# Kernel optimization log

Measured on AMD Instinct MI355X. Metric: run time of the kernel, lower is better.

Reference implementation:

```python
import jax, jax.numpy as jnp
import numpy as np

NH = 12  # attention heads (bert-base)


def _ln(x, s, b, eps=1e-12):
    mu = x.mean(-1, keepdims=True)
    var = ((x - mu) ** 2).mean(-1, keepdims=True)
    return (x - mu) / jnp.sqrt(var + eps) * s + b


def _forward(input_ids, token_type_ids, attention_mask, word_emb, pos_emb, type_emb,
             emb_ln_s, emb_ln_b, memory, q_w, q_b, k_w, k_b, v_w, v_b, o_w, o_b,
             ln1_s, ln1_b, f_w1, f_b1, f_w2, f_b2, ln2_s, ln2_b,
             key_w1, key_b1, key_w2, key_b2, val_w1, val_b1, val_w2, val_b2):
    B, S = input_ids.shape
    M, H = memory.shape
    T = S + M
    m = attention_mask.astype(jnp.int32)          # [B,S] 0/1
    L = m.sum(-1)                                 # [B] number of real tokens
    tok_emb = word_emb[input_ids]                 # [B,S,H]
    # stable argsort puts mask==1 positions first (in original order), then mask==0
    order = jnp.argsort(1 - m, axis=-1)           # [B,S]
    p = jnp.arange(T)[None, :]                    # [1,T]
    Lb = L[:, None]
    # output layout per sample: [real tokens (L), memory (M), pad tokens (S-L)]
    src_p = jnp.clip(jnp.where(p < Lb, p, p - M), 0, S - 1)
    src_idx = jnp.take_along_axis(order, src_p, axis=1)                  # [B,T]
    gathered = jnp.take_along_axis(tok_emb, src_idx[..., None], axis=1)  # [B,T,H]
    is_mem = (p >= Lb) & (p < Lb + M)
    mem_idx = jnp.clip(p - Lb, 0, M - 1)
    emb = jnp.where(is_mem[..., None], memory[mem_idx], gathered)        # spliced embeds
    att = (p < Lb + M).astype(emb.dtype)                                 # [B,T]
    tt = jnp.where(p < Lb, jnp.take_along_axis(token_type_ids.astype(jnp.int32), src_idx, axis=1), 1)
    # --- BERT encoder on inputs_embeds ---
    x = _ln(emb + pos_emb[None, :T] + type_emb[tt], emb_ln_s, emb_ln_b)
    bias = ((1.0 - att) * -10000.0)[:, None, None, :]                    # [B,1,1,T]
    dh = H // NH
    for l in range(q_w.shape[0]):
        q = (x @ q_w[l] + q_b[l]).reshape(B, T, NH, dh)
        k = (x @ k_w[l] + k_b[l]).reshape(B, T, NH, dh)
        v = (x @ v_w[l] + v_b[l]).reshape(B, T, NH, dh)
        s = jnp.einsum('bqhd,bkhd->bhqk', q, k) / jnp.sqrt(jnp.asarray(dh, x.dtype)) + bias
        a = jax.nn.softmax(s, axis=-1)
        ctx = jnp.einsum('bhqk,bkhd->bqhd', a, v).reshape(B, T, H)
        x = _ln(x + ctx @ o_w[l] + o_b[l], ln1_s[l], ln1_b[l])
        h = jax.nn.gelu(x @ f_w1[l] + f_b1[l], approximate=False)
        x = _ln(x + h @ f_w2[l] + f_b2[l], ln2_s[l], ln2_b[l])
    # --- gated key/value softmax pooling (get_rep_no_vae) ---
    value = jnp.tanh(jax.nn.relu(x @ val_w1 + val_b1) @ val_w2 + val_b2)       # [B,T,E]
    weight = jax.nn.sigmoid(jax.nn.relu(x @ key_w1 + key_b1) @ key_w2 + key_b2)  # [B,T,E]
    pool_mask = jnp.where(tt == 1, -jnp.inf, 0.0).astype(x.dtype)[..., None]   # [B,T,1]
    fw = jax.nn.softmax(weight + pool_mask, axis=-2)  # softmax over token dim
    return jax.nn.relu((fw * value).sum(-2))          # [B,E]


def setup_inputs() -> dict:
    key = jax.random.key(0)
    ks = jax.random.split(key, 20)
    B, S, M, H, E, V, NL, FF = 8, 512, 64, 768, 512, 30522, 2, 3072
    def rn(k, shape, s=0.02):
        return jax.random.normal(k, shape, jnp.float32) * s
    return {
        'input_ids': jax.random.randint(ks[0], (B, S), 0, V),
        'token_type_ids': jnp.zeros((B, S), jnp.int32),
        'attention_mask': jax.random.randint(ks[1], (B, S), 0, 2),
        'word_emb': rn(ks[2], (V, H)),
        'pos_emb': rn(ks[3], (S + M, H)),
        'type_emb': rn(ks[4], (2, H)),
        'emb_ln_s': jnp.ones((H,), jnp.float32), 'emb_ln_b': jnp.zeros((H,), jnp.float32),
        'memory': rn(ks[5], (M, H), 1.0),
        'q_w': rn(ks[6], (NL, H, H)), 'q_b': jnp.zeros((NL, H), jnp.float32),
        'k_w': rn(ks[7], (NL, H, H)), 'k_b': jnp.zeros((NL, H), jnp.float32),
        'v_w': rn(ks[8], (NL, H, H)), 'v_b': jnp.zeros((NL, H), jnp.float32),
        'o_w': rn(ks[9], (NL, H, H)), 'o_b': jnp.zeros((NL, H), jnp.float32),
        'ln1_s': jnp.ones((NL, H), jnp.float32), 'ln1_b': jnp.zeros((NL, H), jnp.float32),
        'f_w1': rn(ks[10], (NL, H, FF)), 'f_b1': jnp.zeros((NL, FF), jnp.float32),
        'f_w2': rn(ks[11], (NL, FF, H)), 'f_b2': jnp.zeros((NL, H), jnp.float32),
        'ln2_s': jnp.ones((NL, H), jnp.float32), 'ln2_b': jnp.zeros((NL, H), jnp.float32),
        'key_w1': rn(ks[12], (H, 2 * H)), 'key_b1': jnp.zeros((2 * H,), jnp.float32),
        'key_w2': rn(ks[13], (2 * H, E)), 'key_b2': jnp.zeros((E,), jnp.float32),
        'val_w1': rn(ks[14], (H, 2 * E)), 'val_b1': jnp.zeros((2 * E,), jnp.float32),
        'val_w2': rn(ks[15], (2 * E, E)), 'val_b2': jnp.zeros((E,), jnp.float32),
    }


def reference(input_ids, token_type_ids, attention_mask, word_emb, pos_emb, type_emb,
              emb_ln_s, emb_ln_b, memory, q_w, q_b, k_w, k_b, v_w, v_b, o_w, o_b,
              ln1_s, ln1_b, f_w1, f_b1, f_w2, f_b2, ln2_s, ln2_b,
              key_w1, key_b1, key_w2, key_b2, val_w1, val_b1, val_w2, val_b2):
    return _forward(input_ids, token_type_ids, attention_mask, word_emb, pos_emb, type_emb,
                    emb_ln_s, emb_ln_b, memory, q_w, q_b, k_w, k_b, v_w, v_b, o_w, o_b,
                    ln1_s, ln1_b, f_w1, f_b1, f_w2, f_b2, ln2_s, ln2_b,
                    key_w1, key_b1, key_w2, key_b2, val_w1, val_b1, val_w2, val_b2)
```

## Files before the change

kernel.cpp:

```cpp
#include <hip/hip_runtime.h>
#include <hip/hip_bf16.h>

#define B 8
#define S 512
#define MM 64
#define T 576
#define H 768
#define NH 12
#define DH 64
#define FF 3072
#define E 512
#define NL 2

typedef __attribute__((ext_vector_type(8))) short bf16x8;
typedef __attribute__((ext_vector_type(4))) float f32x4;

__device__ inline unsigned short bf16_rne(float f) {
    unsigned u = __builtin_bit_cast(unsigned, f);
    unsigned r = u + 0x7FFFu + ((u >> 16) & 1u);
    return (unsigned short)(r >> 16);
}

__device__ inline f32x4 mfma16(bf16x8 a, bf16x8 b, f32x4 c) {
    return __builtin_amdgcn_mfma_f32_16x16x32_bf16(a, b, c, 0, 0, 0);
}

__device__ inline void load_lds16(const void* g, void* l) {
    __builtin_amdgcn_global_load_lds((const __attribute__((address_space(1))) void*)g,
                                     (__attribute__((address_space(3))) void*)l, 16, 0, 0);
}

__global__ void order_kernel(const int* __restrict__ mask, int* __restrict__ ord,
                             int* __restrict__ Larr) {
    __shared__ int ps[S];
    int b = blockIdx.x;
    int t = threadIdx.x;
    int mv = (mask[b * S + t] != 0) ? 1 : 0;
    ps[t] = mv;
    __syncthreads();
    for (int off = 1; off < S; off <<= 1) {
        int v = ps[t];
        int add = (t >= off) ? ps[t - off] : 0;
        __syncthreads();
        ps[t] = v + add;
        __syncthreads();
    }
    int L = ps[S - 1];
    int rank = mv ? (ps[t] - 1) : (L + (t - ps[t]));
    ord[b * S + rank] = t;
    if (t == 0) Larr[b] = L;
}

__global__ void scan_kernel(const int* __restrict__ Larr, int* __restrict__ boff,
                            int* __restrict__ rowb) {
    __shared__ int sb[B + 1];
    if (threadIdx.x == 0) {
        int acc = 0;
        for (int b = 0; b < B; ++b) { sb[b] = acc; boff[b] = acc; acc += Larr[b] + MM; }
        sb[B] = acc; boff[B] = acc;
    }
    __syncthreads();
    for (int r = threadIdx.x; r < B * T; r += blockDim.x) {
        int bb = 0;
        #pragma unroll
        for (int b2 = 1; b2 < B; ++b2) bb += (r >= sb[b2]) ? 1 : 0;
        rowb[r] = bb;
    }
}

__global__ void embed_kernel(const int* __restrict__ ids, const int* __restrict__ toktype,
                             const int* __restrict__ ord, const int* __restrict__ Larr,
                             const int* __restrict__ boff,
                             const float* __restrict__ word_emb, const float* __restrict__ pos_emb,
                             const float* __restrict__ type_emb, const float* __restrict__ memory,
                             const float* __restrict__ lns, const float* __restrict__ lnb,
                             float* __restrict__ x, unsigned short* __restrict__ xb,
                             int* __restrict__ ttarr) {
    int t = blockIdx.x;
    int b = blockIdx.y;
    int Lb = Larr[b];
    if (t >= Lb + MM) return;
    int row = boff[b] + t;
    int tid = threadIdx.x;
    int tt;
    const float* src;
    if (t < Lb) {
        int sp = ord[b * S + t];
        tt = toktype[b * S + sp];
        src = &word_emb[(size_t)ids[b * S + sp] * H];
    } else {
        tt = 1;
        src = &memory[(size_t)(t - Lb) * H];
    }
    __shared__ float rowv[H];
    __shared__ float r1[256], r2[256];
    float lsum = 0.f, lsq = 0.f;
    for (int hh = tid; hh < H; hh += 256) {
        float v = src[hh] + pos_emb[(size_t)t * H + hh] + type_emb[(size_t)tt * H + hh];
        rowv[hh] = v;
        lsum += v;
        lsq += v * v;
    }
    r1[tid] = lsum; r2[tid] = lsq;
    __syncthreads();
    for (int s = 128; s > 0; s >>= 1) {
        if (tid < s) { r1[tid] += r1[tid + s]; r2[tid] += r2[tid + s]; }
        __syncthreads();
    }
    float mu = r1[0] / H;
    float var = r2[0] / H - mu * mu;
    float inv = rsqrtf(var + 1e-12f);
    for (int hh = tid; hh < H; hh += 256) {
        float v = (rowv[hh] - mu) * inv * lns[hh] + lnb[hh];
        x[(size_t)row * H + hh] = v;
        xb[(size_t)row * H + hh] = bf16_rne(v);
    }
    if (tid == 0) ttarr[row] = tt;
}

#define ACT_NONE 0
#define ACT_RELU 1
#define ACT_GELU 2
#define ACT_SIGMOID 3
#define ACT_TANH 4

template <int ACT>
__device__ inline float apply_act(float v) {
    if constexpr (ACT == ACT_RELU) return fmaxf(v, 0.f);
    else if constexpr (ACT == ACT_GELU) {
        float y = v * 0.70710678118654752f;
        float a = fabsf(y);
        float t = 1.f / (1.f + 0.3275911f * a);
        float poly = t * (0.254829592f + t * (-0.284496736f + t * (1.421413741f +
                     t * (-1.453152027f + t * 1.061405429f))));
        float e = poly * exp2f(-a * a * 1.4426950408889634f);
        float erfv = 1.f - e;
        erfv = (y < 0.f) ? -erfv : erfv;
        return 0.5f * v * (1.f + erfv);
    }
    else if constexpr (ACT == ACT_SIGMOID) return 1.f / (1.f + expf(-v));
    else if constexpr (ACT == ACT_TANH) return tanhf(v);
    else return v;
}

struct TDesc { const float* src; unsigned dstoff; int Kd; int Nd; int tile0; };
struct TTab { TDesc d[10]; int n; };

__global__ __launch_bounds__(256) void transpose_all(TTab tab, unsigned short* __restrict__ dstbase) {
    int tile = blockIdx.x;
    int mi = 0;
    #pragma unroll
    for (int i = 1; i < 10; ++i)
        if (i < tab.n && tab.d[i].tile0 <= tile) mi = i;
    TDesc d = tab.d[mi];
    int rel = tile - d.tile0;
    int tilesK = d.Kd >> 5;
    int kt = rel % tilesK, nt = rel / tilesK;
    __shared__ float ts[32][33];
    int k0 = kt * 32, n0 = nt * 32;
    int tx = threadIdx.x & 31, ty = threadIdx.x >> 5;
    #pragma unroll
    for (int r = 0; r < 4; ++r) {
        int kk = ty + r * 8;
        ts[kk][tx] = d.src[(size_t)(k0 + kk) * d.Nd + n0 + tx];
    }
    __syncthreads();
    unsigned short* Wt = dstbase + d.dstoff;
    #pragma unroll
    for (int r = 0; r < 4; ++r) {
        int nn = ty + r * 8;
        Wt[(size_t)(n0 + nn) * d.Kd + k0 + tx] = bf16_rne(ts[tx][nn]);
    }
}

#define EPI_F32   0
#define EPI_BF16  1
#define EPI_QKV   2
#define EPI_SPLIT2 3

template <int ACT, int EPI, int NSPLIT>
__global__ __launch_bounds__(256) void mfma_gemm(
    const unsigned short* __restrict__ A, const unsigned short* __restrict__ Bt,
    const float* __restrict__ b0, const float* __restrict__ b1, const float* __restrict__ b2,
    int sp1, int sp2,
    float* __restrict__ Cf, float* __restrict__ Cf2,
    unsigned short* __restrict__ Cb, unsigned short* __restrict__ Cb2,
    unsigned short* __restrict__ Vt, int n2w,
    const int* __restrict__ boffs, const int* __restrict__ rowb,
    int Mdim, int Ndim, int Kdim) {
    __shared__ unsigned short As[2][128 * 32];
    __shared__ unsigned short Bs[2][128 * 32];

    const int bn = blockIdx.x * 128, bm = blockIdx.y * 128;

    const int Mtot = boffs[B];
    if (bm >= Mtot) return;

    const int z = (NSPLIT > 1) ? blockIdx.z : 0;
    const int Klocal = Kdim / NSPLIT;
    const int koff = z * Klocal;

    const int tid = threadIdx.x;
    const int w = tid >> 6, lane = tid & 63;
    const int lr = lane & 15, g = lane >> 4;
    const int wr = w >> 1, wc = w & 1;
    f32x4 acc[4][4] = {};

    const int srow = w * 32 + (lane >> 2);
    const int kc = (((lane & 3) ^ ((lane >> 4) & 3)) * 8);
    const unsigned short* ga0 = A + (size_t)(bm + srow) * Kdim + kc;
    const unsigned short* ga1 = A + (size_t)(bm + srow + 16) * Kdim + kc;
    const unsigned short* gb0 = Bt + (size_t)(bn + srow) * Kdim + kc;
    const unsigned short* gb1 = Bt + (size_t)(bn + srow + 16) * Kdim + kc;
    const int d0 = (w * 32) * 32, d1 = (w * 32 + 16) * 32;

    const int sw = ((g ^ ((lr >> 2) & 3)) & 3) * 8;

    auto stage = [&](int pp, int k0) {
        load_lds16(ga0 + k0, &As[pp][d0]);
        load_lds16(ga1 + k0, &As[pp][d1]);
        load_lds16(gb0 + k0, &Bs[pp][d0]);
        load_lds16(gb1 + k0, &Bs[pp][d1]);
    };
    auto compute = [&](int pp) {
        bf16x8 af[4], bfr[4];
        #pragma unroll
        for (int i = 0; i < 4; ++i)
            af[i] = *(const bf16x8*)&As[pp][(wr * 64 + i * 16 + lr) * 32 + sw];
        #pragma unroll
        for (int j = 0; j < 4; ++j)
            bfr[j] = *(const bf16x8*)&Bs[pp][(wc * 64 + j * 16 + lr) * 32 + sw];
        __builtin_amdgcn_s_setprio(1);
        #pragma unroll
        for (int i = 0; i < 4; ++i)
            #pragma unroll
            for (int j = 0; j < 4; ++j)
                acc[i][j] = mfma16(af[i], bfr[j], acc[i][j]);
        __builtin_amdgcn_s_setprio(0);
    };

    const int nk = Klocal >> 5;
    stage(0, koff);
    int p = 0;
    for (int s = 0; s < nk; ++s) {
        if (s + 1 < nk) {
            stage(p ^ 1, koff + (s + 1) * 32);
            asm volatile("s_waitcnt vmcnt(4)" ::: "memory");
        } else {
            asm volatile("s_waitcnt vmcnt(0)" ::: "memory");
        }
        __builtin_amdgcn_s_barrier();
        __builtin_amdgcn_sched_barrier(0);
        compute(p);
        __builtin_amdgcn_sched_barrier(0);
        __builtin_amdgcn_s_barrier();
        __builtin_amdgcn_sched_barrier(0);
        p ^= 1;
    }

    float* Cdst = (NSPLIT > 1 && z == 1) ? Cf2 : Cf;
    #pragma unroll
    for (int i = 0; i < 4; ++i) {
        const int row0 = bm + wr * 64 + i * 16 + 4 * g;
        #pragma unroll
        for (int j = 0; j < 4; ++j) {
            const int col = bn + wc * 64 + j * 16 + lr;
            float bv = (NSPLIT > 1 && z == 1) ? 0.f
                     : ((col < sp1) ? b0[col] : (col < sp2 ? b1[col - sp1] : b2[col - sp2]));
            float vv[4];
            #pragma unroll
            for (int r = 0; r < 4; ++r) vv[r] = apply_act<ACT>(acc[i][j][r] + bv);
            if constexpr (EPI == EPI_F32) {
                #pragma unroll
                for (int r = 0; r < 4; ++r) Cdst[(size_t)(row0 + r) * Ndim + col] = vv[r];
            } else if constexpr (EPI == EPI_BF16) {
                #pragma unroll
                for (int r = 0; r < 4; ++r) Cb[(size_t)(row0 + r) * Ndim + col] = bf16_rne(vv[r]);
            } else if constexpr (EPI == EPI_QKV) {
                if (col < 1536) {
                    #pragma unroll
                    for (int r = 0; r < 4; ++r) Cb[(size_t)(row0 + r) * 1536 + col] = bf16_rne(vv[r]);
                } else {
                    int c2 = col - 1536;
                    int hh2 = c2 >> 6, dd = c2 & 63;
                    int bb = rowb[row0];
                    if (row0 + 3 < Mtot && rowb[row0 + 3] == bb) {
                        int t0 = row0 - boffs[bb];
                        unsigned lo = (unsigned)bf16_rne(vv[0]) | ((unsigned)bf16_rne(vv[1]) << 16);
                        unsigned hi = (unsigned)bf16_rne(vv[2]) | ((unsigned)bf16_rne(vv[3]) << 16);
                        size_t idxv = (((size_t)bb * NH + hh2) * DH + dd) * T + t0;
                        *(uint2*)&Vt[idxv] = make_uint2(lo, hi);
                    } else {
                        #pragma unroll
                        for (int r = 0; r < 4; ++r) {
                            int rr = row0 + r;
                            if (rr < Mtot) {
                                int b2 = rowb[rr];
                                int t2 = rr - boffs[b2];
                                Vt[(((size_t)b2 * NH + hh2) * DH + dd) * T + t2] = bf16_rne(vv[r]);
                            }
                        }
                    }
                }
            } else {
                if (col < sp1) {
                    #pragma unroll
                    for (int r = 0; r < 4; ++r) Cb[(size_t)(row0 + r) * sp1 + col] = bf16_rne(vv[r]);
                } else {
                    #pragma unroll
                    for (int r = 0; r < 4; ++r)
                        Cb2[(size_t)(row0 + r) * n2w + (col - sp1)] = bf16_rne(vv[r]);
                }
            }
        }
    }
}

#define C2 0.180336880111116670f
#define MB2 14426.950408889634f

__global__ __launch_bounds__(256) void attn_mfma(
    const unsigned short* __restrict__ QK, const unsigned short* __restrict__ Vt,
    const int* __restrict__ Larr, const int* __restrict__ boffs,
    unsigned short* __restrict__ ctxb) {
    const int n = blockIdx.x;
    const int xcd = n & 7, k = n >> 3;
    const int p = xcd * 12 + k / 9, qt = k % 9;
    const int b = p / NH, h = p % NH;
    const int LbMM = Larr[b] + MM;
    if (qt * 64 >= LbMM) return;
    const int w = threadIdx.x >> 6, lane = threadIdx.x & 63;
    const int q0 = qt * 64 + w * 16;
    if (q0 >= LbMM) return;
    const int base = boffs[b];
    const int lr = lane & 15, g = lane >> 4;
    __shared__ unsigned short P[4][16][72];
    const unsigned short* qrow = QK + (size_t)(base + q0 + lr) * 1536 + h * 64;
    bf16x8 qf0 = *(const bf16x8*)(qrow + 8 * g);
    bf16x8 qf1 = *(const bf16x8*)(qrow + 32 + 8 * g);
    f32x4 ctx[4] = {};
    float m_run = -1e30f, l_run = 0.f;
    const size_t vbase = ((size_t)b * NH + h) * DH;
    for (int kt = 0; kt < LbMM; kt += 64) {
        f32x4 sf[4];
        #pragma unroll
        for (int i = 0; i < 4; ++i) {
            const unsigned short* krow =
                QK + (size_t)(base + kt + 16 * i + lr) * 1536 + 768 + h * 64;
            bf16x8 kf0 = *(const bf16x8*)(krow + 8 * g);
            bf16x8 kf1 = *(const bf16x8*)(krow + 32 + 8 * g);
            f32x4 s = {};
            s = mfma16(kf0, qf0, s);
            s = mfma16(kf1, qf1, s);
            sf[i] = s;
        }
        float tmax = -1e30f;
        #pragma unroll
        for (int i = 0; i < 4; ++i)
            #pragma unroll
            for (int r = 0; r < 4; ++r) {
                int key = kt + 16 * i + 4 * g + r;
                float v = sf[i][r] * C2 + (key < LbMM ? 0.f : -MB2);
                sf[i][r] = v;
                tmax = fmaxf(tmax, v);
            }
        tmax = fmaxf(tmax, __shfl_xor(tmax, 16));
        tmax = fmaxf(tmax, __shfl_xor(tmax, 32));
        float m_new = fmaxf(m_run, tmax);
        float scale = exp2f(m_run - m_new);
        m_run = m_new;
        float psum = 0.f;
        #pragma unroll
        for (int i = 0; i < 4; ++i)
            #pragma unroll
            for (int r = 0; r < 4; ++r) {
                float pv = exp2f(sf[i][r] - m_new);
                sf[i][r] = pv;
                psum += pv;
            }
        l_run = l_run * scale + psum;
        float f0 = __shfl(scale, 4 * g + 0);
        float f1 = __shfl(scale, 4 * g + 1);
        float f2 = __shfl(scale, 4 * g + 2);
        float f3 = __shfl(scale, 4 * g + 3);
        #pragma unroll
        for (int j = 0; j < 4; ++j) {
            ctx[j][0] *= f0; ctx[j][1] *= f1; ctx[j][2] *= f2; ctx[j][3] *= f3;
        }
        #pragma unroll
        for (int i = 0; i < 4; ++i) {
            unsigned lo = (unsigned)bf16_rne(sf[i][0]) | ((unsigned)bf16_rne(sf[i][1]) << 16);
            unsigned hi = (unsigned)bf16_rne(sf[i][2]) | ((unsigned)bf16_rne(sf[i][3]) << 16);
            *(unsigned*)&P[w][lr][16 * i + 4 * g] = lo;
            *(unsigned*)&P[w][lr][16 * i + 4 * g + 2] = hi;
        }
        asm volatile("s_waitcnt lgkmcnt(0)" ::: "memory");
        __builtin_amdgcn_sched_barrier(0);
        #pragma unroll
        for (int s2 = 0; s2 < 2; ++s2) {
            bf16x8 pa = *(const bf16x8*)&P[w][lr][32 * s2 + 8 * g];
            #pragma unroll
            for (int j = 0; j < 4; ++j) {
                const unsigned short* vrow =
                    Vt + (vbase + 16 * j + lr) * T + kt + 32 * s2 + 8 * g;
                bf16x8 vf = *(const bf16x8*)vrow;
                ctx[j] = mfma16(pa, vf, ctx[j]);
            }
        }
        asm volatile("s_waitcnt lgkmcnt(0)" ::: "memory");
        __builtin_amdgcn_sched_barrier(0);
    }
    l_run += __shfl_xor(l_run, 16);
    l_run += __shfl_xor(l_run, 32);
    float inv = 1.f / l_run;
    float i0 = __shfl(inv, 4 * g + 0);
    float i1 = __shfl(inv, 4 * g + 1);
    float i2 = __shfl(inv, 4 * g + 2);
    float i3 = __shfl(inv, 4 * g + 3);
    float sc[4] = {i0, i1, i2, i3};
    #pragma unroll
    for (int j = 0; j < 4; ++j)
        #pragma unroll
        for (int r = 0; r < 4; ++r) {
            int rl = q0 + 4 * g + r;
            if (rl < LbMM)
                ctxb[(size_t)(base + rl) * H + h * 64 + 16 * j + lr] =
                    bf16_rne(ctx[j][r] * sc[r]);
        }
}

__global__ void lnres_kernel(float* __restrict__ x, const float* __restrict__ d1,
                             const float* __restrict__ d2,
                             const float* __restrict__ s, const float* __restrict__ bvec,
                             unsigned short* __restrict__ xb, const int* __restrict__ mtotp) {
    int r = blockIdx.x;
    if (r >= mtotp[0]) return;
    int tid = threadIdx.x;
    __shared__ float4 row[H / 4];
    __shared__ float r1[256], r2[256];
    float lsum = 0.f, lsq = 0.f;
    size_t off4 = (size_t)r * (H / 4);
    const float4* x4 = (const float4*)x;
    const float4* d14 = (const float4*)d1;
    const float4* d24 = (const float4*)d2;
    if (tid < H / 4) {
        float4 a = x4[off4 + tid], bb = d14[off4 + tid], cc = d24[off4 + tid];
        float4 v = make_float4(a.x + bb.x + cc.x, a.y + bb.y + cc.y,
                               a.z + bb.z + cc.z, a.w + bb.w + cc.w);
        row[tid] = v;
        lsum = v.x + v.y + v.z + v.w;
        lsq = v.x * v.x + v.y * v.y + v.z * v.z + v.w * v.w;
    }
    r1[tid] = lsum; r2[tid] = lsq;
    __syncthreads();
    for (int ss = 128; ss > 0; ss >>= 1) {
        if (tid < ss) { r1[tid] += r1[tid + ss]; r2[tid] += r2[tid + ss]; }
        __syncthreads();
    }
    float mu = r1[0] / H;
    float var = r2[0] / H - mu * mu;
    float inv = rsqrtf(var + 1e-12f);
    if (tid < H / 4) {
        float4 v = row[tid];
        const float4 sv = ((const float4*)s)[tid];
        const float4 bv = ((const float4*)bvec)[tid];
        float4 o = make_float4((v.x - mu) * inv * sv.x + bv.x,
                               (v.y - mu) * inv * sv.y + bv.y,
                               (v.z - mu) * inv * sv.z + bv.z,
                               (v.w - mu) * inv * sv.w + bv.w);
        ((float4*)x)[off4 + tid] = o;
        ushort4 ob = make_ushort4(bf16_rne(o.x), bf16_rne(o.y), bf16_rne(o.z), bf16_rne(o.w));
        *(ushort4*)&xb[(size_t)r * H + tid * 4] = ob;
    }
}

__global__ __launch_bounds__(256) void pool_kernel(
    const float* __restrict__ w0, const float* __restrict__ w1,
    const float* __restrict__ value, const int* __restrict__ ttarr,
    const int* __restrict__ boffs, float* __restrict__ out) {
    int b = blockIdx.x;
    int le = threadIdx.x & 31;
    int e = blockIdx.y * 32 + le;
    int tg = threadIdx.x >> 5;
    int base = boffs[b];
    int nrow = boffs[b + 1] - base;
    __shared__ int ttl[T];
    __shared__ float red[8][33];
    for (int t = threadIdx.x; t < nrow; t += 256) ttl[t] = ttarr[base + t];
    __syncthreads();
    float mx = -1e30f;
    for (int t = tg; t < nrow; t += 8) {
        if (ttl[t] == 1) continue;
        size_t idx = (size_t)(base + t) * E + e;
        float w = 1.f / (1.f + expf(-(w0[idx] + w1[idx])));
        mx = fmaxf(mx, w);
    }
    red[tg][le] = mx;
    __syncthreads();
    #pragma unroll
    for (int i = 0; i < 8; ++i) mx = fmaxf(mx, red[i][le]);
    float den = 0.f, num = 0.f;
    for (int t = tg; t < nrow; t += 8) {
        if (ttl[t] == 1) continue;
        size_t idx = (size_t)(base + t) * E + e;
        float w = 1.f / (1.f + expf(-(w0[idx] + w1[idx])));
        float ew = expf(w - mx);
        den += ew;
        num = fmaf(ew, value[idx], num);
    }
    __syncthreads();
    red[tg][le] = den;
    __syncthreads();
    float dtot = 0.f;
    #pragma unroll
    for (int i = 0; i < 8; ++i) dtot += red[i][le];
    __syncthreads();
    red[tg][le] = num;
    __syncthreads();
    float ntot = 0.f;
    #pragma unroll
    for (int i = 0; i < 8; ++i) ntot += red[i][le];
    if (tg == 0) out[(size_t)b * E + e] = fmaxf(ntot / dtot, 0.f);
}

extern "C" void kernel_launch(void* const* d_in, const int* in_sizes, int n_in,
                              void* d_out, int out_size, void* d_ws, size_t ws_size,
                              hipStream_t stream) {
    const int*   input_ids  = (const int*)d_in[0];
    const int*   token_type = (const int*)d_in[1];
    const int*   attn_mask  = (const int*)d_in[2];
    const float* word_emb   = (const float*)d_in[3];
    const float* pos_emb    = (const float*)d_in[4];
    const float* type_emb   = (const float*)d_in[5];
    const float* emb_ln_s   = (const float*)d_in[6];
    const float* emb_ln_b   = (const float*)d_in[7];
    const float* memory     = (const float*)d_in[8];
    const float* q_w  = (const float*)d_in[9];
    const float* q_b  = (const float*)d_in[10];
    const float* k_w  = (const float*)d_in[11];
    const float* k_b  = (const float*)d_in[12];
    const float* v_w  = (const float*)d_in[13];
    const float* v_b  = (const float*)d_in[14];
    const float* o_w  = (const float*)d_in[15];
    const float* o_b  = (const float*)d_in[16];
    const float* ln1_s = (const float*)d_in[17];
    const float* ln1_b = (const float*)d_in[18];
    const float* f_w1  = (const float*)d_in[19];
    const float* f_b1  = (const float*)d_in[20];
    const float* f_w2  = (const float*)d_in[21];
    const float* f_b2  = (const float*)d_in[22];
    const float* ln2_s = (const float*)d_in[23];
    const float* ln2_b = (const float*)d_in[24];
    const float* key_w1 = (const float*)d_in[25];
    const float* key_b1 = (const float*)d_in[26];
    const float* key_w2 = (const float*)d_in[27];
    const float* key_b2 = (const float*)d_in[28];
    const float* val_w1 = (const float*)d_in[29];
    const float* val_b1 = (const float*)d_in[30];
    const float* val_w2 = (const float*)d_in[31];
    const float* val_b2 = (const float*)d_in[32];
    float* out = (float*)d_out;

    char* ws = (char*)d_ws;
    size_t off = 0;
    auto alloc = [&](size_t bytes) {
        void* p = ws + off;
        off += (bytes + 255) & ~(size_t)255;
        return p;
    };
    const size_t BT  = (size_t)B * T;
    const size_t BTH = BT * H;

    int*   ord   = (int*)alloc((size_t)B * S * 4);
    int*   Larr  = (int*)alloc(64);
    int*   boff  = (int*)alloc((B + 1) * 4);
    int*   rowb  = (int*)alloc(BT * 4);
    int*   ttarr = (int*)alloc(BT * 4);
    float* x     = (float*)alloc(BTH * 4);
    unsigned short* xb   = (unsigned short*)alloc(BTH * 2);
    unsigned short* reg1 = (unsigned short*)alloc(BT * FF * 2);
    float* Bbuf  = (float*)alloc(BTH * 4);
    float* part1 = (float*)alloc(BTH * 4);
    unsigned short* wt = (unsigned short*)alloc((size_t)10354688 * 2);

    unsigned short* qkb  = reg1;
    unsigned short* Vtb  = reg1 + BT * 1536;
    unsigned short* ctxb = reg1 + BT * 1536 + BTH;
    unsigned short* hb   = reg1;
    unsigned short* key1b = reg1;
    unsigned short* val1b = reg1 + BT * 1536;
    float* valf = x;

    unsigned short* wt_qkv = wt;
    unsigned short* wt_o  = wt + (size_t)2304 * 768;
    unsigned short* wt_f1 = wt_o + (size_t)768 * 768;
    unsigned short* wt_f2 = wt_f1 + (size_t)3072 * 768;
    unsigned short* wt_head = wt + (size_t)7077888;
    unsigned short* wt_kv1 = wt_head;
    unsigned short* wt_k2 = wt_head + (size_t)2560 * 768;
    unsigned short* wt_v2 = wt_k2 + (size_t)512 * 1536;

    const int Mrows = (int)BT;
    const size_t HH = (size_t)H * H;
    const int BIG = 1 << 30;
    const int* mtotp = boff + B;

    hipLaunchKernelGGL(order_kernel, dim3(B), dim3(S), 0, stream, attn_mask, ord, Larr);
    hipLaunchKernelGGL(scan_kernel, dim3(1), dim3(256), 0, stream, Larr, boff, rowb);
    hipLaunchKernelGGL(embed_kernel, dim3(T, B), dim3(256), 0, stream,
                       input_ids, token_type, ord, Larr, boff, word_emb, pos_emb, type_emb,
                       memory, emb_ln_s, emb_ln_b, x, xb, ttarr);

    for (int l = 0; l < NL; ++l) {
        TTab tab;
        tab.d[0] = { q_w + l * HH,              0u,                              H,  H,  0    };
        tab.d[1] = { k_w + l * HH,              (unsigned)(768 * 768),           H,  H,  576  };
        tab.d[2] = { v_w + l * HH,              (unsigned)(1536 * 768),          H,  H,  1152 };
        tab.d[3] = { o_w + l * HH,              (unsigned)(2304 * 768),          H,  H,  1728 };
        tab.d[4] = { f_w1 + (size_t)l * H * FF, (unsigned)(3072 * 768),          H,  FF, 2304 };
        tab.d[5] = { f_w2 + (size_t)l * FF * H, (unsigned)(6144 * 768),          FF, H,  4608 };
        int ntiles = 6912;
        if (l == NL - 1) {
            tab.d[6] = { key_w1, 7077888u,                     H,     2 * H, 6912 };
            tab.d[7] = { val_w1, 7077888u + 1536u * 768u,      H,     2 * E, 8064 };
            tab.d[8] = { key_w2, 9043968u,                     2 * H, E,     8832 };
            tab.d[9] = { val_w2, 9830400u,                     2 * E, E,     9600 };
            tab.n = 10;
            ntiles = 10112;
        } else {
            tab.n = 6;
        }
        hipLaunchKernelGGL(transpose_all, dim3(ntiles), dim3(256), 0, stream, tab, wt);

        mfma_gemm<ACT_NONE, EPI_QKV, 1><<<dim3(18, 36), 256, 0, stream>>>(
            xb, wt_qkv, q_b + (size_t)l * H, k_b + (size_t)l * H, v_b + (size_t)l * H,
            768, 1536, nullptr, nullptr, qkb, nullptr, Vtb, 0, boff, rowb, Mrows, 2304, H);
        hipLaunchKernelGGL(attn_mfma, dim3(864), dim3(256), 0, stream,
                           qkb, Vtb, Larr, boff, ctxb);
        mfma_gemm<ACT_NONE, EPI_F32, 2><<<dim3(6, 36, 2), 256, 0, stream>>>(
            ctxb, wt_o, o_b + (size_t)l * H, nullptr, nullptr, BIG, BIG,
            Bbuf, part1, nullptr, nullptr, nullptr, 0, boff, rowb, Mrows, H, H);
        hipLaunchKernelGGL(lnres_kernel, dim3((int)BT), dim3(256), 0, stream,
                           x, Bbuf, part1, ln1_s + (size_t)l * H, ln1_b + (size_t)l * H, xb, mtotp);
        mfma_gemm<ACT_GELU, EPI_BF16, 1><<<dim3(24, 36), 256, 0, stream>>>(
            xb, wt_f1, f_b1 + (size_t)l * FF, nullptr, nullptr, BIG, BIG,
            nullptr, nullptr, hb, nullptr, nullptr, 0, boff, rowb, Mrows, FF, H);
        mfma_gemm<ACT_NONE, EPI_F32, 2><<<dim3(6, 36, 2), 256, 0, stream>>>(
            hb, wt_f2, f_b2 + (size_t)l * H, nullptr, nullptr, BIG, BIG,
            Bbuf, part1, nullptr, nullptr, nullptr, 0, boff, rowb, Mrows, H, FF);
        hipLaunchKernelGGL(lnres_kernel, dim3((int)BT), dim3(256), 0, stream,
                           x, Bbuf, part1, ln2_s + (size_t)l * H, ln2_b + (size_t)l * H, xb, mtotp);
    }

    mfma_gemm<ACT_RELU, EPI_SPLIT2, 1><<<dim3(20, 36), 256, 0, stream>>>(
        xb, wt_kv1, key_b1, val_b1, nullptr, 1536, BIG,
        nullptr, nullptr, key1b, val1b, nullptr, 1024, boff, rowb, Mrows, 2560, H);
    mfma_gemm<ACT_NONE, EPI_F32, 2><<<dim3(4, 36, 2), 256, 0, stream>>>(
        key1b, wt_k2, key_b2, nullptr, nullptr, BIG, BIG,
        Bbuf, part1, nullptr, nullptr, nullptr, 0, boff, rowb, Mrows, 512, 1536);
    mfma_gemm<ACT_TANH, EPI_F32, 1><<<dim3(4, 36), 256, 0, stream>>>(
        val1b, wt_v2, val_b2, nullptr, nullptr, BIG, BIG,
        valf, nullptr, nullptr, nullptr, nullptr, 0, boff, rowb, Mrows, 512, 1024);
    hipLaunchKernelGGL(pool_kernel, dim3(B, E / 32), dim3(256), 0, stream,
                       Bbuf, part1, valf, ttarr, boff, out);
}
```

Before: 500.5 us.

## Split-K by four on narrow GEMMs and hoist all weight transposes into one launch

The output-projection, FFN-down and head GEMMs now split K four ways instead of two (or not at all for the value head). The four fp32 partials are summed inside the residual-LayerNorm and pooling kernels, and the value-head tanh moves into pooling. The intent is to fill more CUs on these narrow-N grids. Weight transposes for both layers and the heads are merged into one launch with a larger buffer, removing a per-layer launch and its serialization. The cost is extra partial-buffer traffic and memory, plus reading four partials in the consumer kernels.

```diff
diff --git a/kernel.cpp b/kernel.cpp
--- a/kernel.cpp
+++ b/kernel.cpp
@@ -144,13 +144,13 @@
 }
 
 struct TDesc { const float* src; unsigned dstoff; int Kd; int Nd; int tile0; };
-struct TTab { TDesc d[10]; int n; };
+struct TTab { TDesc d[16]; int n; };
 
 __global__ __launch_bounds__(256) void transpose_all(TTab tab, unsigned short* __restrict__ dstbase) {
     int tile = blockIdx.x;
     int mi = 0;
     #pragma unroll
-    for (int i = 1; i < 10; ++i)
+    for (int i = 1; i < 16; ++i)
         if (i < tab.n && tab.d[i].tile0 <= tile) mi = i;
     TDesc d = tab.d[mi];
     int rel = tile - d.tile0;
@@ -184,6 +184,7 @@
     const float* __restrict__ b0, const float* __restrict__ b1, const float* __restrict__ b2,
     int sp1, int sp2,
     float* __restrict__ Cf, float* __restrict__ Cf2,
+    float* __restrict__ Cf3, float* __restrict__ Cf4,
     unsigned short* __restrict__ Cb, unsigned short* __restrict__ Cb2,
     unsigned short* __restrict__ Vt, int n2w,
     const int* __restrict__ boffs, const int* __restrict__ rowb,
@@ -258,14 +259,14 @@
         p ^= 1;
     }
 
-    float* Cdst = (NSPLIT > 1 && z == 1) ? Cf2 : Cf;
+    float* Cdst = (z == 0) ? Cf : (z == 1) ? Cf2 : (z == 2) ? Cf3 : Cf4;
     #pragma unroll
     for (int i = 0; i < 4; ++i) {
         const int row0 = bm + wr * 64 + i * 16 + 4 * g;
         #pragma unroll
         for (int j = 0; j < 4; ++j) {
             const int col = bn + wc * 64 + j * 16 + lr;
-            float bv = (NSPLIT > 1 && z == 1) ? 0.f
+            float bv = (NSPLIT > 1 && z != 0) ? 0.f
                      : ((col < sp1) ? b0[col] : (col < sp2 ? b1[col - sp1] : b2[col - sp2]));
             float vv[4];
             #pragma unroll
@@ -430,7 +431,8 @@
 }
 
 __global__ void lnres_kernel(float* __restrict__ x, const float* __restrict__ d1,
-                             const float* __restrict__ d2,
+                             const float* __restrict__ d2, const float* __restrict__ d3,
+                             const float* __restrict__ d4,
                              const float* __restrict__ s, const float* __restrict__ bvec,
                              unsigned short* __restrict__ xb, const int* __restrict__ mtotp) {
     int r = blockIdx.x;
@@ -440,13 +442,16 @@
     __shared__ float r1[256], r2[256];
     float lsum = 0.f, lsq = 0.f;
     size_t off4 = (size_t)r * (H / 4);
-    const float4* x4 = (const float4*)x;
-    const float4* d14 = (const float4*)d1;
-    const float4* d24 = (const float4*)d2;
     if (tid < H / 4) {
-        float4 a = x4[off4 + tid], bb = d14[off4 + tid], cc = d24[off4 + tid];
-        float4 v = make_float4(a.x + bb.x + cc.x, a.y + bb.y + cc.y,
-                               a.z + bb.z + cc.z, a.w + bb.w + cc.w);
+        float4 a = ((const float4*)x)[off4 + tid];
+        float4 p1 = ((const float4*)d1)[off4 + tid];
+        float4 p2 = ((const float4*)d2)[off4 + tid];
+        float4 p3 = ((const float4*)d3)[off4 + tid];
+        float4 p4 = ((const float4*)d4)[off4 + tid];
+        float4 v = make_float4(a.x + p1.x + p2.x + p3.x + p4.x,
+                               a.y + p1.y + p2.y + p3.y + p4.y,
+                               a.z + p1.z + p2.z + p3.z + p4.z,
+                               a.w + p1.w + p2.w + p3.w + p4.w);
         row[tid] = v;
         lsum = v.x + v.y + v.z + v.w;
         lsq = v.x * v.x + v.y * v.y + v.z * v.z + v.w * v.w;
@@ -476,8 +481,11 @@
 
 __global__ __launch_bounds__(256) void pool_kernel(
     const float* __restrict__ w0, const float* __restrict__ w1,
-    const float* __restrict__ value, const int* __restrict__ ttarr,
-    const int* __restrict__ boffs, float* __restrict__ out) {
+    const float* __restrict__ w2, const float* __restrict__ w3,
+    const float* __restrict__ v0, const float* __restrict__ v1,
+    const float* __restrict__ v2, const float* __restrict__ v3,
+    const int* __restrict__ ttarr, const int* __restrict__ boffs,
+    float* __restrict__ out) {
     int b = blockIdx.x;
     int le = threadIdx.x & 31;
     int e = blockIdx.y * 32 + le;
@@ -492,7 +500,7 @@
     for (int t = tg; t < nrow; t += 8) {
         if (ttl[t] == 1) continue;
         size_t idx = (size_t)(base + t) * E + e;
-        float w = 1.f / (1.f + expf(-(w0[idx] + w1[idx])));
+        float w = 1.f / (1.f + expf(-(w0[idx] + w1[idx] + w2[idx] + w3[idx])));
         mx = fmaxf(mx, w);
     }
     red[tg][le] = mx;
@@ -503,10 +511,11 @@
     for (int t = tg; t < nrow; t += 8) {
         if (ttl[t] == 1) continue;
         size_t idx = (size_t)(base + t) * E + e;
-        float w = 1.f / (1.f + expf(-(w0[idx] + w1[idx])));
+        float w = 1.f / (1.f + expf(-(w0[idx] + w1[idx] + w2[idx] + w3[idx])));
+        float vval = tanhf(v0[idx] + v1[idx] + v2[idx] + v3[idx]);
         float ew = expf(w - mx);
         den += ew;
-        num = fmaf(ew, value[idx], num);
+        num = fmaf(ew, vval, num);
     }
     __syncthreads();
     red[tg][le] = den;
@@ -579,9 +588,15 @@
     float* x     = (float*)alloc(BTH * 4);
     unsigned short* xb   = (unsigned short*)alloc(BTH * 2);
     unsigned short* reg1 = (unsigned short*)alloc(BT * FF * 2);
-    float* Bbuf  = (float*)alloc(BTH * 4);
-    float* part1 = (float*)alloc(BTH * 4);
-    unsigned short* wt = (unsigned short*)alloc((size_t)10354688 * 2);
+    float* P0 = (float*)alloc(BTH * 4);
+    float* P1 = (float*)alloc(BTH * 4);
+    float* P2 = (float*)alloc(BTH * 4);
+    float* P3 = (float*)alloc(BTH * 4);
+    float* V0 = (float*)alloc(BT * E * 4);
+    float* V1 = (float*)alloc(BT * E * 4);
+    float* V2 = (float*)alloc(BT * E * 4);
+    float* V3 = (float*)alloc(BT * E * 4);
+    unsigned short* wt = (unsigned short*)alloc((size_t)17432576 * 2);
 
     unsigned short* qkb  = reg1;
     unsigned short* Vtb  = reg1 + BT * 1536;
@@ -589,13 +604,8 @@
     unsigned short* hb   = reg1;
     unsigned short* key1b = reg1;
     unsigned short* val1b = reg1 + BT * 1536;
-    float* valf = x;
-
-    unsigned short* wt_qkv = wt;
-    unsigned short* wt_o  = wt + (size_t)2304 * 768;
-    unsigned short* wt_f1 = wt_o + (size_t)768 * 768;
-    unsigned short* wt_f2 = wt_f1 + (size_t)3072 * 768;
-    unsigned short* wt_head = wt + (size_t)7077888;
+
+    unsigned short* wt_head = wt + (size_t)14155776;
     unsigned short* wt_kv1 = wt_head;
     unsigned short* wt_k2 = wt_head + (size_t)2560 * 768;
     unsigned short* wt_v2 = wt_k2 + (size_t)512 * 1536;
@@ -607,60 +617,72 @@
 
     hipLaunchKernelGGL(order_kernel, dim3(B), dim3(S), 0, stream, attn_mask, ord, Larr);
     hipLaunchKernelGGL(scan_kernel, dim3(1), dim3(256), 0, stream, Larr, boff, rowb);
+
+    {
+        TTab tab;
+        tab.n = 16;
+        for (int l = 0; l < NL; ++l) {
+            unsigned base = (unsigned)(l * 7077888);
+            int t0 = l * 6912;
+            tab.d[l * 6 + 0] = { q_w + l * HH,              base,                        H,  H,  t0        };
+            tab.d[l * 6 + 1] = { k_w + l * HH,              base + 768u * 768u,          H,  H,  t0 + 576  };
+            tab.d[l * 6 + 2] = { v_w + l * HH,              base + 1536u * 768u,         H,  H,  t0 + 1152 };
+            tab.d[l * 6 + 3] = { o_w + l * HH,              base + 2304u * 768u,         H,  H,  t0 + 1728 };
+            tab.d[l * 6 + 4] = { f_w1 + (size_t)l * H * FF, base + 3072u * 768u,         H,  FF, t0 + 2304 };
+            tab.d[l * 6 + 5] = { f_w2 + (size_t)l * FF * H, base + 6144u * 768u,         FF, H,  t0 + 4608 };
+        }
+        tab.d[12] = { key_w1, 14155776u,                    H,     2 * H, 13824 };
+        tab.d[13] = { val_w1, 14155776u + 1536u * 768u,     H,     2 * E, 14976 };
+        tab.d[14] = { key_w2, 16121856u,                    2 * H, E,     15744 };
+        tab.d[15] = { val_w2, 16908288u,                    2 * E, E,     16512 };
+        hipLaunchKernelGGL(transpose_all, dim3(17024), dim3(256), 0, stream, tab, wt);
+    }
+
     hipLaunchKernelGGL(embed_kernel, dim3(T, B), dim3(256), 0, stream,
                        input_ids, token_type, ord, Larr, boff, word_emb, pos_emb, type_emb,
                        memory, emb_ln_s, emb_ln_b, x, xb, ttarr);
 
     for (int l = 0; l < NL; ++l) {
-        TTab tab;
-        tab.d[0] = { q_w + l * HH,              0u,                              H,  H,  0    };
-        tab.d[1] = { k_w + l * HH,              (unsigned)(768 * 768),           H,  H,  576  };
-        tab.d[2] = { v_w + l * HH,              (unsigned)(1536 * 768),          H,  H,  1152 };
-        tab.d[3] = { o_w + l * HH,              (unsigned)(2304 * 768),          H,  H,  1728 };
-        tab.d[4] = { f_w1 + (size_t)l * H * FF, (unsigned)(3072 * 768),          H,  FF, 2304 };
-        tab.d[5] = { f_w2 + (size_t)l * FF * H, (unsigned)(6144 * 768),          FF, H,  4608 };
-        int ntiles = 6912;
-        if (l == NL - 1) {
-            tab.d[6] = { key_w1, 7077888u,                     H,     2 * H, 6912 };
-            tab.d[7] = { val_w1, 7077888u + 1536u * 768u,      H,     2 * E, 8064 };
-            tab.d[8] = { key_w2, 9043968u,                     2 * H, E,     8832 };
-            tab.d[9] = { val_w2, 9830400u,                     2 * E, E,     9600 };
-            tab.n = 10;
-            ntiles = 10112;
-        } else {
-            tab.n = 6;
-        }
-        hipLaunchKernelGGL(transpose_all, dim3(ntiles), dim3(256), 0, stream, tab, wt);
+        unsigned short* wt_l   = wt + (size_t)l * 7077888;
+        unsigned short* wt_qkv = wt_l;
+        unsigned short* wt_o   = wt_l + (size_t)2304 * 768;
+        unsigned short* wt_f1  = wt_o + (size_t)768 * 768;
+        unsigned short* wt_f2  = wt_f1 + (size_t)3072 * 768;
 
         mfma_gemm<ACT_NONE, EPI_QKV, 1><<<dim3(18, 36), 256, 0, stream>>>(
             xb, wt_qkv, q_b + (size_t)l * H, k_b + (size_t)l * H, v_b + (size_t)l * H,
-            768, 1536, nullptr, nullptr, qkb, nullptr, Vtb, 0, boff, rowb, Mrows, 2304, H);
+            768, 1536, nullptr, nullptr, nullptr, nullptr, qkb, nullptr, Vtb, 0,
+            boff, rowb, Mrows, 2304, H);
         hipLaunchKernelGGL(attn_mfma, dim3(864), dim3(256), 0, stream,
                            qkb, Vtb, Larr, boff, ctxb);
-        mfma_gemm<ACT_NONE, EPI_F32, 2><<<dim3(6, 36, 2), 256, 0, stream>>>(
+        mfma_gemm<ACT_NONE, EPI_F32, 4><<<dim3(6, 36, 4), 256, 0, stream>>>(
             ctxb, wt_o, o_b + (size_t)l * H, nullptr, nullptr, BIG, BIG,
-            Bbuf, part1, nullptr, nullptr, nullptr, 0, boff, rowb, Mrows, H, H);
+            P0, P1, P2, P3, nullptr, nullptr, nullptr, 0, boff, rowb, Mrows, H, H);
         hipLaunchKernelGGL(lnres_kernel, dim3((int)BT), dim3(256), 0, stream,
-                           x, Bbuf, part1, ln1_s + (size_t)l * H, ln1_b + (size_t)l * H, xb, mtotp);
+                           x, P0, P1, P2, P3, ln1_s + (size_t)l * H, ln1_b + (size_t)l * H,
+                           xb, mtotp);
         mfma_gemm<ACT_GELU, EPI_BF16, 1><<<dim3(24, 36), 256, 0, stream>>>(
             xb, wt_f1, f_b1 + (size_t)l * FF, nullptr, nullptr, BIG, BIG,
-            nullptr, nullptr, hb, nullptr, nullptr, 0, boff, rowb, Mrows, FF, H);
-        mfma_gemm<ACT_NONE, EPI_F32, 2><<<dim3(6, 36, 2), 256, 0, stream>>>(
+            nullptr, nullptr, nullptr, nullptr, hb, nullptr, nullptr, 0,
+            boff, rowb, Mrows, FF, H);
+        mfma_gemm<ACT_NONE, EPI_F32, 4><<<dim3(6, 36, 4), 256, 0, stream>>>(
             hb, wt_f2, f_b2 + (size_t)l * H, nullptr, nullptr, BIG, BIG,
-            Bbuf, part1, nullptr, nullptr, nullptr, 0, boff, rowb, Mrows, H, FF);
+            P0, P1, P2, P3, nullptr, nullptr, nullptr, 0, boff, rowb, Mrows, H, FF);
         hipLaunchKernelGGL(lnres_kernel, dim3((int)BT), dim3(256), 0, stream,
-                           x, Bbuf, part1, ln2_s + (size_t)l * H, ln2_b + (size_t)l * H, xb, mtotp);
+                           x, P0, P1, P2, P3, ln2_s + (size_t)l * H, ln2_b + (size_t)l * H,
+                           xb, mtotp);
     }
 
     mfma_gemm<ACT_RELU, EPI_SPLIT2, 1><<<dim3(20, 36), 256, 0, stream>>>(
         xb, wt_kv1, key_b1, val_b1, nullptr, 1536, BIG,
-        nullptr, nullptr, key1b, val1b, nullptr, 1024, boff, rowb, Mrows, 2560, H);
-    mfma_gemm<ACT_NONE, EPI_F32, 2><<<dim3(4, 36, 2), 256, 0, stream>>>(
+        nullptr, nullptr, nullptr, nullptr, key1b, val1b, nullptr, 1024,
+        boff, rowb, Mrows, 2560, H);
+    mfma_gemm<ACT_NONE, EPI_F32, 4><<<dim3(4, 36, 4), 256, 0, stream>>>(
         key1b, wt_k2, key_b2, nullptr, nullptr, BIG, BIG,
-        Bbuf, part1, nullptr, nullptr, nullptr, 0, boff, rowb, Mrows, 512, 1536);
-    mfma_gemm<ACT_TANH, EPI_F32, 1><<<dim3(4, 36), 256, 0, stream>>>(
+        P0, P1, P2, P3, nullptr, nullptr, nullptr, 0, boff, rowb, Mrows, 512, 1536);
+    mfma_gemm<ACT_NONE, EPI_F32, 4><<<dim3(4, 36, 4), 256, 0, stream>>>(
         val1b, wt_v2, val_b2, nullptr, nullptr, BIG, BIG,
-        valf, nullptr, nullptr, nullptr, nullptr, 0, boff, rowb, Mrows, 512, 1024);
+        V0, V1, V2, V3, nullptr, nullptr, nullptr, 0, boff, rowb, Mrows, 512, 1024);
     hipLaunchKernelGGL(pool_kernel, dim3(B, E / 32), dim3(256), 0, stream,
-                       Bbuf, part1, valf, ttarr, boff, out);
-}
+                       P0, P1, P2, P3, V0, V1, V2, V3, ttarr, boff, out);
+}
```

After: 474.7 us. -5.2%, faster.
